# Optimization experiments

Hardware: AMD Instinct MI355X
Metric: run time of the kernel (lower is better)

The kernel has to match this reference:

```python
import jax, jax.numpy as jnp
import numpy as np

H = 8
D = 64
SCALER = 1.0 / np.sqrt(D).astype(np.float32)


def setup_inputs() -> dict:
    key = jax.random.key(0)
    k1, k2 = jax.random.split(key)
    B, N, C = 2, 256, 512
    x = jax.random.normal(k1, (B, N, C), dtype=jnp.float32)
    # Linear(C, 5C, bias=False): weight shape [5C, C], torch convention y = x @ W.T
    w = jax.random.normal(k2, (5 * C, C), dtype=jnp.float32) * 0.02
    return {"x": x, "w": w}


def reference(x, w):
    B, N, C = x.shape
    # projections: a, b, c, vj, vk each [B, H, N, D]
    wx = (x @ w.T).reshape(B, N, 5, H, D).transpose(2, 0, 3, 1, 4)
    a, b, c, vj, vk = wx[0], wx[1], wx[2], wx[3], wx[4]

    # three pairwise score matrices, each [B, H, N, N]
    X = jnp.einsum('bhjd,bhkd->bhjk', b, c) * SCALER
    Y = jnp.einsum('bhkd,bhid->bhki', c, a) * SCALER
    Z = jnp.einsum('bhid,bhjd->bhij', a, b) * SCALER

    # custom 3-way softmax stabilization: X uses global max over (j,k),
    # Y uses max over k (axis -2), Z uses max over j (axis -1)
    X = jnp.exp(X - jnp.max(X, axis=(-2, -1), keepdims=True))
    Y = jnp.exp(Y - jnp.max(Y, axis=-2, keepdims=True))
    Z = jnp.exp(Z - jnp.max(Z, axis=-1, keepdims=True))

    # Num_{bhid} = sum_{j,k} Z_ij * X_jk * vj_jd * Y_ki * vk_kd
    # (same math as the original 5D 'bhjkd'/'bhikd' chain, fused via einsum path)
    Num = jnp.einsum('bhij,bhjk,bhjd,bhki,bhkd->bhid', Z, X, vj, Y, vk)
    # Den_{bhi} = sum_{j,k} Z_ij * Y_ki * X_jk
    Den = jnp.einsum('bhij,bhki,bhjk->bhi', Z, Y, X) + 1e-9

    att = Num / Den[..., None]                     # [B, H, N, D]
    att = att.transpose(0, 2, 1, 3).reshape(B, N, C)
    return att
```

## Files before the change

### kernel.cpp

```cpp
#include <hip/hip_runtime.h>
#include <math.h>

#define Bn 2
#define Hn 8
#define Nn 256
#define Dn 64
#define BH 16
#define SCALER 0.125f

typedef _Float16 half8 __attribute__((ext_vector_type(8)));
typedef _Float16 half4 __attribute__((ext_vector_type(4)));
typedef float floatx4 __attribute__((ext_vector_type(4)));

__device__ __forceinline__ void split_f32(float v, _Float16& h, _Float16& l) {
    h = (_Float16)v;
    l = (_Float16)(v - (float)h);
}

__device__ __forceinline__ void split8(const float4& v0, const float4& v1,
                                       half8& h, half8& l) {
    const float vv[8] = {v0.x, v0.y, v0.z, v0.w, v1.x, v1.y, v1.z, v1.w};
    #pragma unroll
    for (int e = 0; e < 8; ++e) {
        _Float16 hh, ll;
        split_f32(vv[e], hh, ll);
        h[e] = hh; l[e] = ll;
    }
}

__device__ __forceinline__ void gload_lds16(const float* g, void* lds_base) {
    __builtin_amdgcn_global_load_lds(
        (const __attribute__((address_space(1))) unsigned int*)g,
        (__attribute__((address_space(3))) unsigned int*)lds_base, 16, 0, 0);
}

__global__ __launch_bounds__(256) void split2_kernel(
    const float* __restrict__ x, const float* __restrict__ w,
    _Float16* __restrict__ xh, _Float16* __restrict__ xl,
    _Float16* __restrict__ wh, _Float16* __restrict__ wl) {
    const int b = blockIdx.x;
    const float* src;
    _Float16 *hp, *lp;
    int idx;
    if (b < 256) {
        idx = (b * 256 + threadIdx.x) * 4;
        src = x; hp = xh; lp = xl;
    } else {
        idx = ((b - 256) * 256 + threadIdx.x) * 4;
        src = w; hp = wh; lp = wl;
    }
    const float4 v = *(const float4*)(src + idx);
    half4 hh, ll;
    _Float16 a2, b2;
    split_f32(v.x, a2, b2); hh[0] = a2; ll[0] = b2;
    split_f32(v.y, a2, b2); hh[1] = a2; ll[1] = b2;
    split_f32(v.z, a2, b2); hh[2] = a2; ll[2] = b2;
    split_f32(v.w, a2, b2); hh[3] = a2; ll[3] = b2;
    *(half4*)(hp + idx) = hh;
    *(half4*)(lp + idx) = ll;
}

__global__ __launch_bounds__(256) void proj_mfma(
    const _Float16* __restrict__ xh, const _Float16* __restrict__ xl,
    const _Float16* __restrict__ wh, const _Float16* __restrict__ wl,
    float* __restrict__ P32, float* __restrict__ vkT) {
    const int m0 = blockIdx.x * 64;
    const int r0 = blockIdx.y * 64;
    const int t = threadIdx.x;
    const int w = t >> 6, l = t & 63;
    const int lr = l & 15, kk8 = (l >> 4) * 8;

    floatx4 acc[4];
    #pragma unroll
    for (int ni = 0; ni < 4; ++ni) acc[ni] = (floatx4){0.f, 0.f, 0.f, 0.f};

    const int arow = m0 + w * 16 + lr;
    for (int kt = 0; kt < 16; ++kt) {
        const int k0 = kt * 32 + kk8;
        const half8 ah = *(const half8*)(xh + arow * 512 + k0);
        const half8 al = *(const half8*)(xl + arow * 512 + k0);
        half8 bhv[4], blv[4];
        #pragma unroll
        for (int ni = 0; ni < 4; ++ni) {
            const int wr = r0 + ni * 16 + lr;
            bhv[ni] = *(const half8*)(wh + wr * 512 + k0);
            blv[ni] = *(const half8*)(wl + wr * 512 + k0);
        }
        #pragma unroll
        for (int ni = 0; ni < 4; ++ni)
            acc[ni] = __builtin_amdgcn_mfma_f32_16x16x32_f16(ah, bhv[ni], acc[ni], 0, 0, 0);
        #pragma unroll
        for (int ni = 0; ni < 4; ++ni)
            acc[ni] = __builtin_amdgcn_mfma_f32_16x16x32_f16(ah, blv[ni], acc[ni], 0, 0, 0);
        #pragma unroll
        for (int ni = 0; ni < 4; ++ni)
            acc[ni] = __builtin_amdgcn_mfma_f32_16x16x32_f16(al, bhv[ni], acc[ni], 0, 0, 0);
    }
    const int rbase = (l >> 4) * 4;
    if (blockIdx.y >= 32) {
        const int mbase = m0 + w * 16 + rbase;
        const int b = mbase >> 8, n = mbase & 255;
        #pragma unroll
        for (int ni = 0; ni < 4; ++ni) {
            const int rcol = r0 + ni * 16 + lr;
            const int h = (rcol >> 6) & 7, d = rcol & 63;
            *(float4*)(vkT + (((b * 8 + h) * 64 + d) * 256 + n)) =
                (float4){acc[ni][0], acc[ni][1], acc[ni][2], acc[ni][3]};
        }
        return;
    }
    #pragma unroll
    for (int ni = 0; ni < 4; ++ni) {
        const int rcol = r0 + ni * 16 + lr;
        const int s = rcol >> 9, h = (rcol >> 6) & 7, d = rcol & 63;
        #pragma unroll
        for (int r = 0; r < 4; ++r) {
            const int m = m0 + w * 16 + rbase + r;
            const int b = m >> 8, n = m & 255;
            P32[(((s * 2 + b) * 8 + h) * 256 + n) * 64 + d] = acc[ni][r];
        }
    }
}

__global__ __launch_bounds__(256) void score_vkt(
    const float* __restrict__ P32,
    _Float16* __restrict__ Xsh, _Float16* __restrict__ Xsl,
    float* __restrict__ Yt, float* __restrict__ Z) {
    const int bh = blockIdx.x, mat = blockIdx.y;
    const int t = threadIdx.x;
    const int i0 = (blockIdx.z >> 2) * 128;
    const int j0 = (blockIdx.z & 3) * 64;
    const int w = t >> 6, l = t & 63;
    const int lr = l & 15, kk8 = (l >> 4) * 8;
    const float* A;
    const float* Bm;
    if (mat == 0)      { A = P32 + (1 * 16 + bh) * 16384; Bm = P32 + (2 * 16 + bh) * 16384; }
    else if (mat == 1) { A = P32 + (0 * 16 + bh) * 16384; Bm = P32 + (2 * 16 + bh) * 16384; }
    else               { A = P32 + (0 * 16 + bh) * 16384; Bm = P32 + (1 * 16 + bh) * 16384; }

    floatx4 acc[2][4];
    #pragma unroll
    for (int mi = 0; mi < 2; ++mi)
        #pragma unroll
        for (int ni = 0; ni < 4; ++ni) acc[mi][ni] = (floatx4){0.f, 0.f, 0.f, 0.f};

    for (int kt = 0; kt < 2; ++kt) {
        const int k0 = kt * 32 + kk8;
        half8 ah[2], al[2], bh8[4], bl8[4];
        #pragma unroll
        for (int mi = 0; mi < 2; ++mi) {
            const int row = i0 + w * 32 + mi * 16 + lr;
            const float4 v0 = *(const float4*)(A + row * 64 + k0);
            const float4 v1 = *(const float4*)(A + row * 64 + k0 + 4);
            split8(v0, v1, ah[mi], al[mi]);
        }
        #pragma unroll
        for (int ni = 0; ni < 4; ++ni) {
            const int row = j0 + ni * 16 + lr;
            const float4 v0 = *(const float4*)(Bm + row * 64 + k0);
            const float4 v1 = *(const float4*)(Bm + row * 64 + k0 + 4);
            split8(v0, v1, bh8[ni], bl8[ni]);
        }
        #pragma unroll
        for (int mi = 0; mi < 2; ++mi)
            #pragma unroll
            for (int ni = 0; ni < 4; ++ni)
                acc[mi][ni] = __builtin_amdgcn_mfma_f32_16x16x32_f16(ah[mi], bh8[ni], acc[mi][ni], 0, 0, 0);
        #pragma unroll
        for (int mi = 0; mi < 2; ++mi)
            #pragma unroll
            for (int ni = 0; ni < 4; ++ni)
                acc[mi][ni] = __builtin_amdgcn_mfma_f32_16x16x32_f16(ah[mi], bl8[ni], acc[mi][ni], 0, 0, 0);
        #pragma unroll
        for (int mi = 0; mi < 2; ++mi)
            #pragma unroll
            for (int ni = 0; ni < 4; ++ni)
                acc[mi][ni] = __builtin_amdgcn_mfma_f32_16x16x32_f16(al[mi], bh8[ni], acc[mi][ni], 0, 0, 0);
    }
    const int rbase = (l >> 4) * 4;
    #pragma unroll
    for (int mi = 0; mi < 2; ++mi)
        #pragma unroll
        for (int ni = 0; ni < 4; ++ni)
            #pragma unroll
            for (int r = 0; r < 4; ++r) {
                const int row = i0 + w * 32 + mi * 16 + rbase + r;
                const int col = j0 + ni * 16 + lr;
                const float e = expf(acc[mi][ni][r] * SCALER);
                if (mat == 0) {
                    const int idx = (bh * 256 + row) * 256 + col;
                    _Float16 hh, ll; split_f32(e, hh, ll);
                    Xsh[idx] = hh; Xsl[idx] = ll;
                } else if (mat == 1) {
                    Yt[bh * 65536 + row * 256 + col] = e;
                } else {
                    Z[bh * 65536 + row * 256 + col] = e;
                }
            }
}

__global__ __launch_bounds__(256) void den_mfma(
    const float* __restrict__ Yt, const _Float16* __restrict__ Xh,
    const _Float16* __restrict__ Xl, const float* __restrict__ Z,
    float* __restrict__ Den) {
    const int bh = blockIdx.x;
    const int ibase = blockIdx.y * 16;
    const int t = threadIdx.x;
    const int w = t >> 6, l = t & 63;
    const int lr = l & 15, ks = l >> 4, kk8 = ks * 8;
    const float* Ytp = Yt + bh * 65536;
    const _Float16* Xhp = Xh + bh * 65536;
    const _Float16* Xlp = Xl + bh * 65536;

    floatx4 acc[4];
    #pragma unroll
    for (int q = 0; q < 4; ++q) acc[q] = (floatx4){0.f, 0.f, 0.f, 0.f};

    for (int kt = 0; kt < 8; ++kt) {
        const int k0 = kt * 32 + kk8;
        half8 ah, al;
        {
            const float4 v0 = *(const float4*)(Ytp + (ibase + lr) * 256 + k0);
            const float4 v1 = *(const float4*)(Ytp + (ibase + lr) * 256 + k0 + 4);
            split8(v0, v1, ah, al);
        }
        half8 bh8[4], bl8[4];
        #pragma unroll
        for (int q = 0; q < 4; ++q) {
            const int jt = w * 4 + q;
            bh8[q] = *(const half8*)(Xhp + (jt * 16 + lr) * 256 + k0);
            bl8[q] = *(const half8*)(Xlp + (jt * 16 + lr) * 256 + k0);
        }
        #pragma unroll
        for (int q = 0; q < 4; ++q)
            acc[q] = __builtin_amdgcn_mfma_f32_16x16x32_f16(ah, bh8[q], acc[q], 0, 0, 0);
        #pragma unroll
        for (int q = 0; q < 4; ++q)
            acc[q] = __builtin_amdgcn_mfma_f32_16x16x32_f16(ah, bl8[q], acc[q], 0, 0, 0);
        #pragma unroll
        for (int q = 0; q < 4; ++q)
            acc[q] = __builtin_amdgcn_mfma_f32_16x16x32_f16(al, bh8[q], acc[q], 0, 0, 0);
    }
    __shared__ float redS[4][16];
    float dp[4] = {0.f, 0.f, 0.f, 0.f};
    const float* Zp = Z + (bh * 256 + ibase) * 256;
    #pragma unroll
    for (int q = 0; q < 4; ++q) {
        const int jt = w * 4 + q;
        #pragma unroll
        for (int r = 0; r < 4; ++r)
            dp[r] += acc[q][r] * Zp[(ks * 4 + r) * 256 + jt * 16 + lr];
    }
    #pragma unroll
    for (int r = 0; r < 4; ++r) {
        float s = dp[r];
        s += __shfl_xor(s, 1); s += __shfl_xor(s, 2);
        s += __shfl_xor(s, 4); s += __shfl_xor(s, 8);
        if (lr == 0) redS[w][ks * 4 + r] = s;
    }
    __syncthreads();
    if (t < 16)
        Den[bh * 256 + ibase + t] =
            redS[0][t] + redS[1][t] + redS[2][t] + redS[3][t] + 1e-9f;
}

__global__ __launch_bounds__(256, 2) void attn_mfma(
    const _Float16* __restrict__ Xh, const _Float16* __restrict__ Xl,
    const float* __restrict__ Yt, const float* __restrict__ Z,
    const float* __restrict__ vkT, const float* __restrict__ P32,
    const float* __restrict__ Den, float* __restrict__ out) {
    const int id = (blockIdx.x & 7) * 256 + (blockIdx.x >> 3);
    const int bh = id >> 7;
    const int i0 = (id & 127) * 2;
    const int t = threadIdx.x;
    const int w = t >> 6, l = t & 63;
    const int lr = l & 15, ks = l >> 4, kk8 = ks * 8;

    __shared__ float yiS[2][256], ziS[2][256];
    __shared__ float RAW[2][2048];
    __shared__ _Float16 BhS[2][2][2048], BlS[2][2][2048];
    float (*redN)[2][64] = reinterpret_cast<float (*)[2][64]>(&yiS[0][0]);

    yiS[0][t] = Yt[(bh * 256 + i0) * 256 + t];
    yiS[1][t] = Yt[(bh * 256 + i0 + 1) * 256 + t];
    ziS[0][t] = Z[(bh * 256 + i0) * 256 + t];
    ziS[1][t] = Z[(bh * 256 + i0 + 1) * 256 + t];

    const _Float16* Xhp = Xh + bh * 65536;
    const _Float16* Xlp = Xl + bh * 65536;
    const float* vkp = vkT + bh * 16384;
    const float* vj = P32 + (3 * 16 + bh) * 16384;

    floatx4 acc[4][8];
    #pragma unroll
    for (int mi = 0; mi < 4; ++mi)
        #pragma unroll
        for (int ct = 0; ct < 8; ++ct) acc[mi][ct] = (floatx4){0.f, 0.f, 0.f, 0.f};

    const int bi = t >> 7;
    const int bd = (t >> 1) & 63;
    const int hf = t & 1;
    const int bs2 = hf * 2;

    auto STAGE = [&](int kt) {
        const int k0 = (kt & 7) * 32;
        const int buf = kt & 1;
        #pragma unroll
        for (int q = 0; q < 2; ++q) {
            const int u = q * 256 + t;
            const int g = u >> 7, ubd = (u & 127) >> 1, uhf = u & 1;
            const float* gp = vkp + ubd * 256 + k0 + uhf * 16 + g * 4;
            void* lp = (char*)&RAW[buf][0] + q * 4096 + w * 1024;
            gload_lds16(gp, lp);
        }
    };
    auto BSTORE = [&](int kt) {
        const int buf = kt & 1;
        const float* yrow = &yiS[bi][(kt & 7) * 32 + bs2 * 8];
        float4 V[4];
        #pragma unroll
        for (int g = 0; g < 4; ++g)
            V[g] = *(float4*)&RAW[buf][g * 512 + bd * 8 + hf * 4];
        #pragma unroll
        for (int g = 0; g < 2; ++g) {
            const float4 y0 = *(const float4*)(yrow + g * 8);
            const float4 y1 = *(const float4*)(yrow + g * 8 + 4);
            const float4 v0 = V[g * 2], v1 = V[g * 2 + 1];
            const float pv[8] = {v0.x * y0.x, v0.y * y0.y, v0.z * y0.z, v0.w * y0.w,
                                 v1.x * y1.x, v1.y * y1.y, v1.z * y1.z, v1.w * y1.w};
            half8 hv, lv;
            #pragma unroll
            for (int e = 0; e < 8; ++e) {
                _Float16 hh, ll;
                split_f32(pv[e], hh, ll);
                hv[e] = hh; lv[e] = ll;
            }
            const int off = ((bd * 4 + bs2 + g) ^ ((bd >> 1) & 7)) * 8;
            *(half8*)&BhS[buf][bi][off] = hv;
            *(half8*)&BlS[buf][bi][off] = lv;
        }
    };
    auto LOADA = [&](half8* AH, half8* AL, int kt) {
        const int k0 = (kt & 7) * 32 + kk8;
        #pragma unroll
        for (int mi = 0; mi < 4; ++mi) {
            const int row = w * 64 + mi * 16 + lr;
            AH[mi] = *(const half8*)(Xhp + row * 256 + k0);
            AL[mi] = *(const half8*)(Xlp + row * 256 + k0);
        }
    };
    auto MFMA_STEP = [&](half8* AH, half8* AL, int buf) {
        __builtin_amdgcn_s_setprio(1);
        #pragma unroll
        for (int ct = 0; ct < 8; ++ct) {
            const int ii = ct >> 2;
            const int dd = (ct & 3) * 16 + lr;
            const int off = ((dd * 4 + ks) ^ ((dd >> 1) & 7)) * 8;
            const half8 bhf = *(const half8*)&BhS[buf][ii][off];
            const half8 blf = *(const half8*)&BlS[buf][ii][off];
            #pragma unroll
            for (int mi = 0; mi < 4; ++mi)
                acc[mi][ct] = __builtin_amdgcn_mfma_f32_16x16x32_f16(AH[mi], bhf, acc[mi][ct], 0, 0, 0);
            #pragma unroll
            for (int mi = 0; mi < 4; ++mi)
                acc[mi][ct] = __builtin_amdgcn_mfma_f32_16x16x32_f16(AH[mi], blf, acc[mi][ct], 0, 0, 0);
            #pragma unroll
            for (int mi = 0; mi < 4; ++mi)
                acc[mi][ct] = __builtin_amdgcn_mfma_f32_16x16x32_f16(AL[mi], bhf, acc[mi][ct], 0, 0, 0);
        }
        __builtin_amdgcn_s_setprio(0);
    };

    half8 A0h[4], A0l[4], A1h[4], A1l[4];

    STAGE(0);
    STAGE(1);
    LOADA(A0h, A0l, 0);
    asm volatile("s_waitcnt vmcnt(10)" ::: "memory");
    __builtin_amdgcn_sched_barrier(0);
    asm volatile("s_waitcnt lgkmcnt(0)" ::: "memory");
    __builtin_amdgcn_s_barrier();
    BSTORE(0);
    asm volatile("s_waitcnt lgkmcnt(0)" ::: "memory");
    __builtin_amdgcn_s_barrier();

    #pragma unroll 1
    for (int kq = 0; kq < 4; ++kq) {
        const int kt = kq * 2;
        STAGE(kt + 2);
        LOADA(A1h, A1l, kt + 1);
        MFMA_STEP(A0h, A0l, 0);
        asm volatile("s_waitcnt vmcnt(18)" ::: "memory");
        __builtin_amdgcn_sched_barrier(0);
        BSTORE(kt + 1);
        asm volatile("s_waitcnt lgkmcnt(0)" ::: "memory");
        __builtin_amdgcn_s_barrier();
        STAGE(kt + 3);
        LOADA(A0h, A0l, kt + 2);
        MFMA_STEP(A1h, A1l, 1);
        if (kq < 3) {
            asm volatile("s_waitcnt vmcnt(18)" ::: "memory");
            __builtin_amdgcn_sched_barrier(0);
            BSTORE(kt + 2);
            asm volatile("s_waitcnt lgkmcnt(0)" ::: "memory");
            __builtin_amdgcn_s_barrier();
        }
    }

    float z0[16], z1[16];
    #pragma unroll
    for (int mi = 0; mi < 4; ++mi)
        #pragma unroll
        for (int r = 0; r < 4; ++r) {
            const int j = w * 64 + mi * 16 + ks * 4 + r;
            z0[mi * 4 + r] = ziS[0][j];
            z1[mi * 4 + r] = ziS[1][j];
        }
    #pragma unroll
    for (int dt = 0; dt < 4; ++dt) {
        float n0 = 0.f, n1 = 0.f;
        #pragma unroll
        for (int mi = 0; mi < 4; ++mi)
            #pragma unroll
            for (int r = 0; r < 4; ++r) {
                const int j = w * 64 + mi * 16 + ks * 4 + r;
                const float v = vj[j * 64 + dt * 16 + lr];
                n0 += acc[mi][dt][r] * z0[mi * 4 + r] * v;
                n1 += acc[mi][dt + 4][r] * z1[mi * 4 + r] * v;
            }
        n0 += __shfl_xor(n0, 16); n0 += __shfl_xor(n0, 32);
        n1 += __shfl_xor(n1, 16); n1 += __shfl_xor(n1, 32);
        if (l < 16) {
            redN[w][0][dt * 16 + l] = n0;
            redN[w][1][dt * 16 + l] = n1;
        }
    }
    __syncthreads();
    if (t < 128) {
        const int ih = t >> 6, d = t & 63;
        const float num = redN[0][ih][d] + redN[1][ih][d] +
                          redN[2][ih][d] + redN[3][ih][d];
        const int i = i0 + ih;
        const float den = Den[bh * 256 + i];
        out[((bh >> 3) * 256 + i) * 512 + (bh & 7) * 64 + d] = num / den;
    }
}

extern "C" void kernel_launch(void* const* d_in, const int* in_sizes, int n_in,
                              void* d_out, int out_size, void* d_ws, size_t ws_size,
                              hipStream_t stream) {
    const float* x = (const float*)d_in[0];
    const float* w = (const float*)d_in[1];
    float* out = (float*)d_out;

    float* ws = (float*)d_ws;
    float* P32 = ws;
    float* U = ws + 1310720;
    _Float16* xh = (_Float16*)U;
    _Float16* xl = xh + 262144;
    _Float16* wh = xl + 262144;
    _Float16* wl = wh + 1310720;
    _Float16* Xsh = (_Float16*)U;
    _Float16* Xsl = Xsh + 1048576;
    float* Yt = U + 1048576;
    float* Z = Yt + 1048576;
    float* vkT = Z + 1048576;
    float* Den = vkT + 262144;

    split2_kernel<<<1536, 256, 0, stream>>>(x, w, xh, xl, wh, wl);
    proj_mfma<<<dim3(8, 40), 256, 0, stream>>>(xh, xl, wh, wl, P32, vkT);
    score_vkt<<<dim3(16, 3, 8), 256, 0, stream>>>(P32, Xsh, Xsl, Yt, Z);
    den_mfma<<<dim3(16, 16), 256, 0, stream>>>(Yt, Xsh, Xsl, Z, Den);
    attn_mfma<<<2048, 256, 0, stream>>>(Xsh, Xsl, Yt, Z, vkT, P32, Den, out);
}
```

Baseline: 180.2 us.

## Process one query row per block in attn_mfma to raise occupancy

Each attn_mfma block now handles a single query row i instead of two, which halves the accumulator registers and LDS tiles, raises the launch bound to 3 blocks per SM and doubles the grid. The hand-tuned vmcnt/lgkmcnt waits and sched barriers are replaced by plain __syncthreads, and the tail STAGE/BSTORE calls are now guarded. In exchange, every block reloads the full X (hi/lo) A-tiles and vkT for only one row, so global and L2 traffic per unit of work roughly doubles.

```diff
diff --git a/kernel.cpp b/kernel.cpp
--- a/kernel.cpp
+++ b/kernel.cpp
@@ -264,47 +264,45 @@
             redS[0][t] + redS[1][t] + redS[2][t] + redS[3][t] + 1e-9f;
 }
 
-__global__ __launch_bounds__(256, 2) void attn_mfma(
+__global__ __launch_bounds__(256, 3) void attn_mfma(
     const _Float16* __restrict__ Xh, const _Float16* __restrict__ Xl,
     const float* __restrict__ Yt, const float* __restrict__ Z,
     const float* __restrict__ vkT, const float* __restrict__ P32,
     const float* __restrict__ Den, float* __restrict__ out) {
-    const int id = (blockIdx.x & 7) * 256 + (blockIdx.x >> 3);
-    const int bh = id >> 7;
-    const int i0 = (id & 127) * 2;
+    const int id = (blockIdx.x & 7) * 512 + (blockIdx.x >> 3);
+    const int bh = id >> 8;
+    const int i = id & 255;
     const int t = threadIdx.x;
     const int w = t >> 6, l = t & 63;
     const int lr = l & 15, ks = l >> 4, kk8 = ks * 8;
 
-    __shared__ float yiS[2][256], ziS[2][256];
+    __shared__ float yiS[256], ziS[256];
     __shared__ float RAW[2][2048];
-    __shared__ _Float16 BhS[2][2][2048], BlS[2][2][2048];
-    float (*redN)[2][64] = reinterpret_cast<float (*)[2][64]>(&yiS[0][0]);
-
-    yiS[0][t] = Yt[(bh * 256 + i0) * 256 + t];
-    yiS[1][t] = Yt[(bh * 256 + i0 + 1) * 256 + t];
-    ziS[0][t] = Z[(bh * 256 + i0) * 256 + t];
-    ziS[1][t] = Z[(bh * 256 + i0 + 1) * 256 + t];
+    __shared__ _Float16 BhS[2][2048], BlS[2][2048];
+    __shared__ float redN[4][64];
+
+    yiS[t] = Yt[(bh * 256 + i) * 256 + t];
+    ziS[t] = Z[(bh * 256 + i) * 256 + t];
 
     const _Float16* Xhp = Xh + bh * 65536;
     const _Float16* Xlp = Xl + bh * 65536;
     const float* vkp = vkT + bh * 16384;
     const float* vj = P32 + (3 * 16 + bh) * 16384;
 
-    floatx4 acc[4][8];
+    floatx4 acc[4][4];
     #pragma unroll
     for (int mi = 0; mi < 4; ++mi)
         #pragma unroll
-        for (int ct = 0; ct < 8; ++ct) acc[mi][ct] = (floatx4){0.f, 0.f, 0.f, 0.f};
-
-    const int bi = t >> 7;
-    const int bd = (t >> 1) & 63;
-    const int hf = t & 1;
-    const int bs2 = hf * 2;
-
-    auto STAGE = [&](int kt) {
-        const int k0 = (kt & 7) * 32;
-        const int buf = kt & 1;
+        for (int ct = 0; ct < 4; ++ct) acc[mi][ct] = (floatx4){0.f, 0.f, 0.f, 0.f};
+
+    const int bd = t >> 2;
+    const int sl = t & 3;
+    const int uhf2 = sl >> 1;
+    const int g0 = (2 * sl) & 3, g1 = (2 * sl + 1) & 3;
+
+    auto STAGE = [&](int kts) {
+        const int k0 = (kts & 7) * 32;
+        const int buf = kts & 1;
         #pragma unroll
         for (int q = 0; q < 2; ++q) {
             const int u = q * 256 + t;
@@ -314,31 +312,25 @@
             gload_lds16(gp, lp);
         }
     };
-    auto BSTORE = [&](int kt) {
-        const int buf = kt & 1;
-        const float* yrow = &yiS[bi][(kt & 7) * 32 + bs2 * 8];
-        float4 V[4];
-        #pragma unroll
-        for (int g = 0; g < 4; ++g)
-            V[g] = *(float4*)&RAW[buf][g * 512 + bd * 8 + hf * 4];
-        #pragma unroll
-        for (int g = 0; g < 2; ++g) {
-            const float4 y0 = *(const float4*)(yrow + g * 8);
-            const float4 y1 = *(const float4*)(yrow + g * 8 + 4);
-            const float4 v0 = V[g * 2], v1 = V[g * 2 + 1];
-            const float pv[8] = {v0.x * y0.x, v0.y * y0.y, v0.z * y0.z, v0.w * y0.w,
-                                 v1.x * y1.x, v1.y * y1.y, v1.z * y1.z, v1.w * y1.w};
-            half8 hv, lv;
-            #pragma unroll
-            for (int e = 0; e < 8; ++e) {
-                _Float16 hh, ll;
-                split_f32(pv[e], hh, ll);
-                hv[e] = hh; lv[e] = ll;
-            }
-            const int off = ((bd * 4 + bs2 + g) ^ ((bd >> 1) & 7)) * 8;
-            *(half8*)&BhS[buf][bi][off] = hv;
-            *(half8*)&BlS[buf][bi][off] = lv;
-        }
+    auto BSTORE = [&](int ktb) {
+        const int buf = ktb & 1;
+        const float* yrow = &yiS[(ktb & 7) * 32 + sl * 8];
+        const float4 v0 = *(float4*)&RAW[buf][(g0 * 128 + bd * 2 + uhf2) * 4];
+        const float4 v1 = *(float4*)&RAW[buf][(g1 * 128 + bd * 2 + uhf2) * 4];
+        const float4 y0 = *(const float4*)(yrow);
+        const float4 y1 = *(const float4*)(yrow + 4);
+        const float pv[8] = {v0.x * y0.x, v0.y * y0.y, v0.z * y0.z, v0.w * y0.w,
+                             v1.x * y1.x, v1.y * y1.y, v1.z * y1.z, v1.w * y1.w};
+        half8 hv, lv;
+        #pragma unroll
+        for (int e = 0; e < 8; ++e) {
+            _Float16 hh, ll;
+            split_f32(pv[e], hh, ll);
+            hv[e] = hh; lv[e] = ll;
+        }
+        const int off = ((bd * 4 + sl) ^ ((bd >> 1) & 7)) * 8;
+        *(half8*)&BhS[buf][off] = hv;
+        *(half8*)&BlS[buf][off] = lv;
     };
     auto LOADA = [&](half8* AH, half8* AL, int kt) {
         const int k0 = (kt & 7) * 32 + kk8;
@@ -352,12 +344,11 @@
     auto MFMA_STEP = [&](half8* AH, half8* AL, int buf) {
         __builtin_amdgcn_s_setprio(1);
         #pragma unroll
-        for (int ct = 0; ct < 8; ++ct) {
-            const int ii = ct >> 2;
-            const int dd = (ct & 3) * 16 + lr;
+        for (int ct = 0; ct < 4; ++ct) {
+            const int dd = ct * 16 + lr;
             const int off = ((dd * 4 + ks) ^ ((dd >> 1) & 7)) * 8;
-            const half8 bhf = *(const half8*)&BhS[buf][ii][off];
-            const half8 blf = *(const half8*)&BlS[buf][ii][off];
+            const half8 bhf = *(const half8*)&BhS[buf][off];
+            const half8 blf = *(const half8*)&BlS[buf][off];
             #pragma unroll
             for (int mi = 0; mi < 4; ++mi)
                 acc[mi][ct] = __builtin_amdgcn_mfma_f32_16x16x32_f16(AH[mi], bhf, acc[mi][ct], 0, 0, 0);
@@ -371,78 +362,54 @@
         __builtin_amdgcn_s_setprio(0);
     };
 
-    half8 A0h[4], A0l[4], A1h[4], A1l[4];
+    half8 Aah[4], Aal[4], Abh[4], Abl[4];
 
     STAGE(0);
     STAGE(1);
-    LOADA(A0h, A0l, 0);
-    asm volatile("s_waitcnt vmcnt(10)" ::: "memory");
-    __builtin_amdgcn_sched_barrier(0);
-    asm volatile("s_waitcnt lgkmcnt(0)" ::: "memory");
-    __builtin_amdgcn_s_barrier();
+    LOADA(Aah, Aal, 0);
+    __syncthreads();
     BSTORE(0);
-    asm volatile("s_waitcnt lgkmcnt(0)" ::: "memory");
-    __builtin_amdgcn_s_barrier();
+    __syncthreads();
 
     #pragma unroll 1
     for (int kq = 0; kq < 4; ++kq) {
         const int kt = kq * 2;
-        STAGE(kt + 2);
-        LOADA(A1h, A1l, kt + 1);
-        MFMA_STEP(A0h, A0l, 0);
-        asm volatile("s_waitcnt vmcnt(18)" ::: "memory");
-        __builtin_amdgcn_sched_barrier(0);
+        if (kt < 6) STAGE(kt + 2);
         BSTORE(kt + 1);
-        asm volatile("s_waitcnt lgkmcnt(0)" ::: "memory");
-        __builtin_amdgcn_s_barrier();
-        STAGE(kt + 3);
-        LOADA(A0h, A0l, kt + 2);
-        MFMA_STEP(A1h, A1l, 1);
-        if (kq < 3) {
-            asm volatile("s_waitcnt vmcnt(18)" ::: "memory");
-            __builtin_amdgcn_sched_barrier(0);
-            BSTORE(kt + 2);
-            asm volatile("s_waitcnt lgkmcnt(0)" ::: "memory");
-            __builtin_amdgcn_s_barrier();
-        }
-    }
-
-    float z0[16], z1[16];
+        LOADA(Abh, Abl, kt + 1);
+        MFMA_STEP(Aah, Aal, 0);
+        __syncthreads();
+        if (kt + 1 < 6) STAGE(kt + 3);
+        if (kt + 1 < 7) BSTORE(kt + 2);
+        LOADA(Aah, Aal, (kt + 2) & 7);
+        MFMA_STEP(Abh, Abl, 1);
+        __syncthreads();
+    }
+
+    float z0[16];
     #pragma unroll
     for (int mi = 0; mi < 4; ++mi)
         #pragma unroll
-        for (int r = 0; r < 4; ++r) {
-            const int j = w * 64 + mi * 16 + ks * 4 + r;
-            z0[mi * 4 + r] = ziS[0][j];
-            z1[mi * 4 + r] = ziS[1][j];
-        }
-    #pragma unroll
-    for (int dt = 0; dt < 4; ++dt) {
-        float n0 = 0.f, n1 = 0.f;
+        for (int r = 0; r < 4; ++r)
+            z0[mi * 4 + r] = ziS[w * 64 + mi * 16 + ks * 4 + r];
+    #pragma unroll
+    for (int ct = 0; ct < 4; ++ct) {
+        float n = 0.f;
         #pragma unroll
         for (int mi = 0; mi < 4; ++mi)
             #pragma unroll
             for (int r = 0; r < 4; ++r) {
                 const int j = w * 64 + mi * 16 + ks * 4 + r;
-                const float v = vj[j * 64 + dt * 16 + lr];
-                n0 += acc[mi][dt][r] * z0[mi * 4 + r] * v;
-                n1 += acc[mi][dt + 4][r] * z1[mi * 4 + r] * v;
+                n += acc[mi][ct][r] * z0[mi * 4 + r] * vj[j * 64 + ct * 16 + lr];
             }
-        n0 += __shfl_xor(n0, 16); n0 += __shfl_xor(n0, 32);
-        n1 += __shfl_xor(n1, 16); n1 += __shfl_xor(n1, 32);
-        if (l < 16) {
-            redN[w][0][dt * 16 + l] = n0;
-            redN[w][1][dt * 16 + l] = n1;
-        }
+        n += __shfl_xor(n, 16); n += __shfl_xor(n, 32);
+        if (l < 16) redN[w][ct * 16 + l] = n;
     }
     __syncthreads();
-    if (t < 128) {
-        const int ih = t >> 6, d = t & 63;
-        const float num = redN[0][ih][d] + redN[1][ih][d] +
-                          redN[2][ih][d] + redN[3][ih][d];
-        const int i = i0 + ih;
+    if (t < 64) {
+        const float num = redN[0][t] + redN[1][t] + redN[2][t] + redN[3][t];
         const float den = Den[bh * 256 + i];
-        out[((bh >> 3) * 256 + i) * 512 + (bh & 7) * 64 + d] = num / den;
+        out[((bh >> 3) * 256 + i) * 512 + (bh & 7) * 64 + t] = num / den;
     }
 }
 
@@ -471,5 +438,5 @@
     proj_mfma<<<dim3(8, 40), 256, 0, stream>>>(xh, xl, wh, wl, P32, vkT);
     score_vkt<<<dim3(16, 3, 8), 256, 0, stream>>>(P32, Xsh, Xsl, Yt, Z);
     den_mfma<<<dim3(16, 16), 256, 0, stream>>>(Yt, Xsh, Xsl, Z, Den);
-    attn_mfma<<<2048, 256, 0, stream>>>(Xsh, Xsl, Yt, Z, vkT, P32, Den, out);
-}
+    attn_mfma<<<4096, 256, 0, stream>>>(Xsh, Xsl, Yt, Z, vkT, P32, Den, out);
+}
```

Measured after the change: 292.1 us. 1.62x slower.

## Stage vk through registers with 64-wide K tiles instead of LDS DMA

Applied to the files above, without the earlier changes.

Replaces the global-to-LDS direct loads of vk (RAW buffer) with per-thread register loads. The k-tile grows from 32 to 64, so the B operand is built once per 64 k and there are four outer iterations with two MFMA sub-steps each, halving the number of barriers. The swizzle of the B LDS layout changes to match the new 64-wide rows. LDS use stays roughly the same, but the vk prefetch now depends on register latency hiding and adds register pressure, with the vmcnt waits retuned.

```diff
diff --git a/kernel.cpp b/kernel.cpp
--- a/kernel.cpp
+++ b/kernel.cpp
@@ -26,12 +26,6 @@
         split_f32(vv[e], hh, ll);
         h[e] = hh; l[e] = ll;
     }
-}
-
-__device__ __forceinline__ void gload_lds16(const float* g, void* lds_base) {
-    __builtin_amdgcn_global_load_lds(
-        (const __attribute__((address_space(1))) unsigned int*)g,
-        (__attribute__((address_space(3))) unsigned int*)lds_base, 16, 0, 0);
 }
 
 __global__ __launch_bounds__(256) void split2_kernel(
@@ -277,8 +271,7 @@
     const int lr = l & 15, ks = l >> 4, kk8 = ks * 8;
 
     __shared__ float yiS[2][256], ziS[2][256];
-    __shared__ float RAW[2][2048];
-    __shared__ _Float16 BhS[2][2][2048], BlS[2][2][2048];
+    __shared__ _Float16 BhS[2][2][4096], BlS[2][2][4096];
     float (*redN)[2][64] = reinterpret_cast<float (*)[2][64]>(&yiS[0][0]);
 
     yiS[0][t] = Yt[(bh * 256 + i0) * 256 + t];
@@ -297,51 +290,43 @@
         #pragma unroll
         for (int ct = 0; ct < 8; ++ct) acc[mi][ct] = (floatx4){0.f, 0.f, 0.f, 0.f};
 
-    const int bi = t >> 7;
-    const int bd = (t >> 1) & 63;
-    const int hf = t & 1;
-    const int bs2 = hf * 2;
-
-    auto STAGE = [&](int kt) {
-        const int k0 = (kt & 7) * 32;
-        const int buf = kt & 1;
-        #pragma unroll
-        for (int q = 0; q < 2; ++q) {
-            const int u = q * 256 + t;
-            const int g = u >> 7, ubd = (u & 127) >> 1, uhf = u & 1;
-            const float* gp = vkp + ubd * 256 + k0 + uhf * 16 + g * 4;
-            void* lp = (char*)&RAW[buf][0] + q * 4096 + w * 1024;
-            gload_lds16(gp, lp);
-        }
+    const int vd = t >> 2;
+    const int sl = t & 3;
+    float4 vkr[4];
+
+    auto VKLOAD = [&](int kt) {
+        const float* gp = vkp + vd * 256 + (kt & 3) * 64 + sl * 16;
+        #pragma unroll
+        for (int q = 0; q < 4; ++q) vkr[q] = *(const float4*)(gp + q * 4);
     };
-    auto BSTORE = [&](int kt) {
-        const int buf = kt & 1;
-        const float* yrow = &yiS[bi][(kt & 7) * 32 + bs2 * 8];
-        float4 V[4];
-        #pragma unroll
-        for (int g = 0; g < 4; ++g)
-            V[g] = *(float4*)&RAW[buf][g * 512 + bd * 8 + hf * 4];
-        #pragma unroll
-        for (int g = 0; g < 2; ++g) {
-            const float4 y0 = *(const float4*)(yrow + g * 8);
-            const float4 y1 = *(const float4*)(yrow + g * 8 + 4);
-            const float4 v0 = V[g * 2], v1 = V[g * 2 + 1];
-            const float pv[8] = {v0.x * y0.x, v0.y * y0.y, v0.z * y0.z, v0.w * y0.w,
-                                 v1.x * y1.x, v1.y * y1.y, v1.z * y1.z, v1.w * y1.w};
-            half8 hv, lv;
-            #pragma unroll
-            for (int e = 0; e < 8; ++e) {
-                _Float16 hh, ll;
-                split_f32(pv[e], hh, ll);
-                hv[e] = hh; lv[e] = ll;
+    auto BSTORE = [&](int ktb) {
+        const int buf = ktb & 1;
+        #pragma unroll
+        for (int i = 0; i < 2; ++i) {
+            const float* yrow = &yiS[i][(ktb & 3) * 64 + sl * 16];
+            #pragma unroll
+            for (int hq = 0; hq < 2; ++hq) {
+                const float4 va = vkr[hq * 2], vb = vkr[hq * 2 + 1];
+                const float4 ya = *(const float4*)(yrow + hq * 8);
+                const float4 yb = *(const float4*)(yrow + hq * 8 + 4);
+                const float pv[8] = {va.x * ya.x, va.y * ya.y, va.z * ya.z, va.w * ya.w,
+                                     vb.x * yb.x, vb.y * yb.y, vb.z * yb.z, vb.w * yb.w};
+                half8 hv, lv;
+                #pragma unroll
+                for (int e = 0; e < 8; ++e) {
+                    _Float16 hh, ll;
+                    split_f32(pv[e], hh, ll);
+                    hv[e] = hh; lv[e] = ll;
+                }
+                const int o = sl * 2 + hq;
+                const int g = vd * 8 + (o ^ (vd & 7));
+                *(half8*)&BhS[buf][i][g * 8] = hv;
+                *(half8*)&BlS[buf][i][g * 8] = lv;
             }
-            const int off = ((bd * 4 + bs2 + g) ^ ((bd >> 1) & 7)) * 8;
-            *(half8*)&BhS[buf][bi][off] = hv;
-            *(half8*)&BlS[buf][bi][off] = lv;
         }
     };
-    auto LOADA = [&](half8* AH, half8* AL, int kt) {
-        const int k0 = (kt & 7) * 32 + kk8;
+    auto LOADA = [&](half8* AH, half8* AL, int kt, int sub) {
+        const int k0 = (kt & 3) * 64 + sub * 32 + kk8;
         #pragma unroll
         for (int mi = 0; mi < 4; ++mi) {
             const int row = w * 64 + mi * 16 + lr;
@@ -349,15 +334,16 @@
             AL[mi] = *(const half8*)(Xlp + row * 256 + k0);
         }
     };
-    auto MFMA_STEP = [&](half8* AH, half8* AL, int buf) {
+    auto MFMA_STEP = [&](half8* AH, half8* AL, int buf, int sub) {
         __builtin_amdgcn_s_setprio(1);
         #pragma unroll
         for (int ct = 0; ct < 8; ++ct) {
             const int ii = ct >> 2;
             const int dd = (ct & 3) * 16 + lr;
-            const int off = ((dd * 4 + ks) ^ ((dd >> 1) & 7)) * 8;
-            const half8 bhf = *(const half8*)&BhS[buf][ii][off];
-            const half8 blf = *(const half8*)&BlS[buf][ii][off];
+            const int o = sub * 4 + ks;
+            const int g = dd * 8 + (o ^ (dd & 7));
+            const half8 bhf = *(const half8*)&BhS[buf][ii][g * 8];
+            const half8 blf = *(const half8*)&BlS[buf][ii][g * 8];
             #pragma unroll
             for (int mi = 0; mi < 4; ++mi)
                 acc[mi][ct] = __builtin_amdgcn_mfma_f32_16x16x32_f16(AH[mi], bhf, acc[mi][ct], 0, 0, 0);
@@ -373,39 +359,30 @@
 
     half8 A0h[4], A0l[4], A1h[4], A1l[4];
 
-    STAGE(0);
-    STAGE(1);
-    LOADA(A0h, A0l, 0);
-    asm volatile("s_waitcnt vmcnt(10)" ::: "memory");
+    VKLOAD(0);
+    LOADA(A0h, A0l, 0, 0);
+    asm volatile("s_waitcnt vmcnt(8)" ::: "memory");
     __builtin_amdgcn_sched_barrier(0);
-    asm volatile("s_waitcnt lgkmcnt(0)" ::: "memory");
-    __builtin_amdgcn_s_barrier();
+    __syncthreads();
     BSTORE(0);
-    asm volatile("s_waitcnt lgkmcnt(0)" ::: "memory");
-    __builtin_amdgcn_s_barrier();
+    __syncthreads();
 
     #pragma unroll 1
-    for (int kq = 0; kq < 4; ++kq) {
-        const int kt = kq * 2;
-        STAGE(kt + 2);
-        LOADA(A1h, A1l, kt + 1);
-        MFMA_STEP(A0h, A0l, 0);
-        asm volatile("s_waitcnt vmcnt(18)" ::: "memory");
+    for (int kt = 0; kt < 3; ++kt) {
+        const int buf = kt & 1;
+        VKLOAD(kt + 1);
+        LOADA(A1h, A1l, kt, 1);
+        MFMA_STEP(A0h, A0l, buf, 0);
+        LOADA(A0h, A0l, kt + 1, 0);
+        MFMA_STEP(A1h, A1l, buf, 1);
+        asm volatile("s_waitcnt vmcnt(16)" ::: "memory");
         __builtin_amdgcn_sched_barrier(0);
         BSTORE(kt + 1);
-        asm volatile("s_waitcnt lgkmcnt(0)" ::: "memory");
-        __builtin_amdgcn_s_barrier();
-        STAGE(kt + 3);
-        LOADA(A0h, A0l, kt + 2);
-        MFMA_STEP(A1h, A1l, 1);
-        if (kq < 3) {
-            asm volatile("s_waitcnt vmcnt(18)" ::: "memory");
-            __builtin_amdgcn_sched_barrier(0);
-            BSTORE(kt + 2);
-            asm volatile("s_waitcnt lgkmcnt(0)" ::: "memory");
-            __builtin_amdgcn_s_barrier();
-        }
-    }
+        __syncthreads();
+    }
+    LOADA(A1h, A1l, 3, 1);
+    MFMA_STEP(A0h, A0l, 1, 0);
+    MFMA_STEP(A1h, A1l, 1, 1);
 
     float z0[16], z1[16];
     #pragma unroll
```

Measured after the change: 169.4 us, median of 2. 1.06x faster.
